# Optimization experiments

Hardware: AMD Instinct MI355X
Metric: run time of the kernel (lower is better)

## Reference

```python
import jax, jax.numpy as jnp
import numpy as np

GROUPS = 4
SF = 2   # scale_factor
K = 3    # filter_k

def conv1x1(x, w, b):
    return jnp.einsum('bchw,oc->bohw', x, w) + b[None, :, None, None]

def grid_sample(img, grid):
    # img: (N,C,H,W); grid: (N,Hg,Wg,2) xy in [-1,1]; bilinear, border padding, align_corners=False
    N, C, H, W = img.shape
    ix = jnp.clip(((grid[..., 0] + 1.0) * W - 1.0) * 0.5, 0.0, W - 1.0)
    iy = jnp.clip(((grid[..., 1] + 1.0) * H - 1.0) * 0.5, 0.0, H - 1.0)
    x0 = jnp.floor(ix); y0 = jnp.floor(iy)
    wx = (ix - x0)[..., None]; wy = (iy - y0)[..., None]
    x0i = x0.astype(jnp.int32); y0i = y0.astype(jnp.int32)
    x1i = jnp.minimum(x0i + 1, W - 1); y1i = jnp.minimum(y0i + 1, H - 1)
    bidx = jnp.arange(N)[:, None, None]
    v00 = img[bidx, :, y0i, x0i]; v01 = img[bidx, :, y0i, x1i]
    v10 = img[bidx, :, y1i, x0i]; v11 = img[bidx, :, y1i, x1i]   # (N,Hg,Wg,C)
    out = (v00 * (1 - wx) * (1 - wy) + v01 * wx * (1 - wy)
           + v10 * (1 - wx) * wy + v11 * wx * wy)
    return jnp.transpose(out, (0, 3, 1, 2))

def def_sample(x, off):
    b, c, h, w = x.shape
    g = GROUPS
    off = off.reshape(b * g, SF, SF, 2, h, w).transpose(0, 4, 1, 5, 2, 3)
    hd, wd = SF * h, SF * w
    off = off.reshape(b * g, hd, wd, 2)
    gy, gx = jnp.meshgrid(jnp.arange(hd, dtype=x.dtype) + 0.5,
                          jnp.arange(wd, dtype=x.dtype) + 0.5, indexing='ij')
    base = jnp.stack([gx, gy], axis=-1)[None]
    grid = 2.0 * (base + off) / jnp.array([wd, hd], dtype=x.dtype) - 1.0
    return grid_sample(x.reshape(b * g, c // g, h, w), grid).reshape(b, c, hd, wd)

def dyn_filter(x, compress, kw, kb):
    b, c, h, w = x.shape
    kern = jax.nn.softmax(conv1x1(compress, kw, kb), axis=1)  # (b,K*K,h,w)
    p = K // 2
    xp = jnp.pad(x, ((0, 0), (0, 0), (p, p), (p, p)))
    patches = jnp.stack([xp[:, :, dy:dy + h, dx:dx + w]
                         for dy in range(K) for dx in range(K)], axis=2)  # (b,c,K*K,h,w)
    return jnp.einsum('bkhw,bckhw->bchw', kern, patches)

def trim_op(x, toff):
    b, c, h, w = x.shape
    g = GROUPS
    off = toff.reshape(b, g, 2, h, w).transpose(0, 1, 3, 4, 2)  # (b,g,h,w,2) xy
    gy, gx = jnp.meshgrid(jnp.arange(h, dtype=x.dtype) + 0.5,
                          jnp.arange(w, dtype=x.dtype) + 0.5, indexing='ij')
    base = jnp.stack([gx, gy], axis=-1)[None, None]
    grid = (2.0 * (base + off) / jnp.array([w, h], dtype=x.dtype) - 1.0).reshape(b * g, h, w, 2)
    return grid_sample(x.reshape(b * g, c // g, h, w), grid).reshape(b, c, h, w)

def setup_inputs():
    key = jax.random.key(0)
    ks = jax.random.split(key, 13)
    C = 256
    oc = GROUPS * SF * SF * 2  # 32
    f = jnp.float32
    return {
        "x": jax.random.normal(ks[0], (4, C, 64, 64), f),
        "def_off_w": jax.random.normal(ks[1], (oc, C), f) * 0.001,
        "def_off_b": jnp.zeros((oc,), f),
        "def_ast_w": jax.random.normal(ks[2], (oc, C), f) * 0.01,
        "def_ast_b": jnp.zeros((oc,), f),
        "comp_w": jax.random.normal(ks[3], (64, C), f) * (1.0 / np.sqrt(C).astype(np.float32)),
        "comp_b": jnp.zeros((64,), f),
        "filt_w": jax.random.normal(ks[4], (K * K, 64), f) * 0.001,
        "filt_b": jnp.zeros((K * K,), f),
        "trim_w": jax.random.normal(ks[5], (GROUPS * 2, 64), f) * 0.001,
        "trim_b": jnp.zeros((GROUPS * 2,), f),
        "trim_ast_w": jax.random.normal(ks[6], (GROUPS * 2, 64), f) * 0.01,
        "trim_ast_b": jnp.zeros((GROUPS * 2,), f),
    }

def reference(x, def_off_w, def_off_b, def_ast_w, def_ast_b, comp_w, comp_b,
              filt_w, filt_b, trim_w, trim_b, trim_ast_w, trim_ast_b):
    off = conv1x1(x, def_off_w, def_off_b) * jax.nn.sigmoid(conv1x1(x, def_ast_w, def_ast_b))
    x_up = def_sample(x, off)                              # (b,c,2h,2w)
    comp = conv1x1(x_up, comp_w, comp_b)                   # (b,64,2h,2w)
    x_filt = dyn_filter(x_up, comp, filt_w, filt_b)
    toff = conv1x1(comp, trim_w, trim_b) * jax.nn.sigmoid(conv1x1(comp, trim_ast_w, trim_ast_b))
    return trim_op(x_filt, toff)
```

## Files before the change

### kernel.cpp

```cpp
#include <hip/hip_runtime.h>
#include <hip/hip_bf16.h>
#include <string.h>

typedef __hip_bfloat16 bf16;
typedef __attribute__((ext_vector_type(8))) short short8;
typedef __attribute__((ext_vector_type(4))) short short4v;
typedef __attribute__((ext_vector_type(4))) float f32x4;

__device__ __forceinline__ float b2f(bf16 v) { return __bfloat162float(v); }
__device__ __forceinline__ bf16  f2b(float v) { return __float2bfloat16(v); }
__device__ __forceinline__ float s2f(short s) {
    return __uint_as_float(((unsigned)(unsigned short)s) << 16);
}
__device__ __forceinline__ short f2s(float v) {
    bf16 t = f2b(v); short s; __builtin_memcpy(&s, &t, 2); return s;
}

#define HWD 16384

__global__ __launch_bounds__(512) void k01_xpose_off(const float* __restrict__ x,
        const float* __restrict__ w_off, const float* __restrict__ b_off,
        const float* __restrict__ w_ast, const float* __restrict__ b_ast,
        bf16* __restrict__ xpm, float* __restrict__ offpm)
{
    __shared__ __align__(16) short tileS[64 * 256];
    const int b = blockIdx.x >> 6;
    const int p0 = (blockIdx.x & 63) << 6;
    const int lane = threadIdx.x & 63;
    const int wave = threadIdx.x >> 6;
    const int n = lane & 15, quad = lane >> 4;
    const int wq = wave & 3;
    const int mh = wave >> 2;

    const int j = (wq << 4) + n, oc = j >> 1, kind = j & 1;
    short8 bfrag[8];
    const float* wrow = (kind ? w_ast : w_off) + oc * 256 + quad * 8;
#pragma unroll
    for (int kc = 0; kc < 8; ++kc) {
        float4 lo = *(const float4*)(wrow + kc * 32);
        float4 hi = *(const float4*)(wrow + kc * 32 + 4);
        short8 f;
        f[0] = f2s(lo.x); f[1] = f2s(lo.y); f[2] = f2s(lo.z); f[3] = f2s(lo.w);
        f[4] = f2s(hi.x); f[5] = f2s(hi.y); f[6] = f2s(hi.z); f[7] = f2s(hi.w);
        bfrag[kc] = f;
    }
    float bias = kind ? b_ast[oc] : b_off[oc];

    {
        const float* xb = x + ((size_t)b << 20);
        const int lp = lane;
#pragma unroll
        for (int gg = 0; gg < 4; ++gg) {
            int cbase = (wave << 5) + (gg << 3);
            short8 pk;
#pragma unroll
            for (int jj = 0; jj < 8; ++jj)
                pk[jj] = f2s(xb[((size_t)(cbase + jj) << 12) + p0 + lp]);
            int slot = (cbase >> 3) ^ (lp & 7);
            *(short8*)&tileS[(lp << 8) + (slot << 3)] = pk;
        }
    }
    __syncthreads();

    {
        short* ob = (short*)xpm + ((size_t)((b << 12) + p0) << 8);
#pragma unroll
        for (int rr = 0; rr < 8; ++rr) {
            int r = (wave << 3) + rr;
            short4v v = *(const short4v*)&tileS[(r << 8)
                        + ((((lane >> 1) ^ (r & 7)) << 3) | ((lane & 1) << 2))];
            *(short4v*)(ob + ((size_t)r << 8) + (lane << 2)) = v;
        }
    }

    float* obase = offpm + ((size_t)(b << 12) << 5);
    f32x4 acc0 = {0.f, 0.f, 0.f, 0.f};
    f32x4 acc1 = {0.f, 0.f, 0.f, 0.f};
#pragma unroll
    for (int kc = 0; kc < 8; ++kc) {
        int slot = (((kc << 2) + quad) ^ (n & 7)) << 3;
        short8 a0 = *(const short8*)&tileS[((mh * 32 + n) << 8) + slot];
        short8 a1 = *(const short8*)&tileS[((mh * 32 + 16 + n) << 8) + slot];
        acc0 = __builtin_amdgcn_mfma_f32_16x16x32_bf16(a0, bfrag[kc], acc0, 0, 0, 0);
        acc1 = __builtin_amdgcn_mfma_f32_16x16x32_bf16(a1, bfrag[kc], acc1, 0, 0, 0);
    }
#pragma unroll
    for (int r = 0; r < 4; ++r) {
        float v0 = acc0[r] + bias;
        float v1 = acc1[r] + bias;
        float p0v = __shfl_xor(v0, 1, 64);
        float p1v = __shfl_xor(v1, 1, 64);
        if (!(n & 1)) {
            int px = p0 + mh * 32 + quad * 4 + r;
            obase[((size_t)px << 5) + oc] = v0 * (1.f / (1.f + expf(-p0v)));
            obase[((size_t)(px + 16) << 5) + oc] = v1 * (1.f / (1.f + expf(-p1v)));
        }
    }
}

__global__ __launch_bounds__(256, 2) void k234_defsample_comp_filter(
        const bf16* __restrict__ xpm, const float* __restrict__ offpm,
        const float* __restrict__ cw, const float* __restrict__ cb,
        const float* __restrict__ fw_g, const float* __restrict__ fb,
        const float* __restrict__ tw, const float* __restrict__ tb,
        const float* __restrict__ taw, const float* __restrict__ tab,
        bf16* __restrict__ xfilt, float* __restrict__ toff)
{
    __shared__ __align__(16) short xupS[100 * 256];
    __shared__ __align__(16) float smc[64][65];
    __shared__ __align__(16) float fwS[64 * 12];
    __shared__ __align__(16) float swS[64 * 16];
    __shared__ __align__(16) short kernS[64][18];

    for (int i = threadIdx.x; i < 64 * 12; i += 256) {
        int c = i / 12, k = i % 12;
        fwS[i] = (k < 9) ? fw_g[k * 64 + c] : 0.f;
    }
    for (int i = threadIdx.x; i < 64 * 16; i += 256) {
        int c = i >> 4, jj = i & 15;
        int oc = jj >> 1, kind = jj & 1;
        swS[i] = kind ? taw[oc * 64 + c] : tw[oc * 64 + c];
    }

    const int b = blockIdx.x >> 8;
    const int tile = blockIdx.x & 255;
    const int ty = tile >> 4, tx = tile & 15;
    const int lane = threadIdx.x & 63;
    const int wave = threadIdx.x >> 6;
    const int n = lane & 15, quad = lane >> 4;
    const int ocb = wave << 4;

    short8 bfrag[8];
    const float* wrow = cw + (ocb + n) * 256 + quad * 8;
#pragma unroll
    for (int kc = 0; kc < 8; ++kc) {
        float4 lo = *(const float4*)(wrow + kc * 32);
        float4 hi = *(const float4*)(wrow + kc * 32 + 4);
        short8 f;
        f[0] = f2s(lo.x); f[1] = f2s(lo.y); f[2] = f2s(lo.z); f[3] = f2s(lo.w);
        f[4] = f2s(hi.x); f[5] = f2s(hi.y); f[6] = f2s(hi.z); f[7] = f2s(hi.w);
        bfrag[kc] = f;
    }
    float bias = cb[ocb + n];

    {
        const short* xsrc = (const short*)xpm + ((size_t)b << 20);
        const int e = lane << 2;
        const int g = lane >> 4;
#pragma unroll 5
        for (int i = 0; i < 25; ++i) {
            int l = wave * 25 + i;
            int lhy = (l * 205) >> 11;
            int lwx = l - lhy * 10;
            int hy = ty * 8 - 1 + lhy;  hy = min(max(hy, 0), 127);
            int wx = tx * 8 - 1 + lwx;  wx = min(max(wx, 0), 127);
            int h = hy >> 1, w = wx >> 1;
            int och = (g << 3) + ((hy & 1) << 2) + ((wx & 1) << 1);
            const float* orow = offpm + ((size_t)((b << 12) + (h << 6) + w) << 5);
            float ox = orow[och], oy = orow[och + 1];
            float ix = (wx + 0.5f + ox) * 0.5f - 0.5f;
            float iy = (hy + 0.5f + oy) * 0.5f - 0.5f;
            ix = fminf(fmaxf(ix, 0.f), 63.f);
            iy = fminf(fmaxf(iy, 0.f), 63.f);
            float x0f = floorf(ix), y0f = floorf(iy);
            float fx = ix - x0f, fy = iy - y0f;
            int x0 = (int)x0f, y0 = (int)y0f;
            int x1 = min(x0 + 1, 63), y1 = min(y0 + 1, 63);
            float w00 = (1.f - fx) * (1.f - fy), w01 = fx * (1.f - fy);
            float w10 = (1.f - fx) * fy,        w11 = fx * fy;
            short4v v00 = *(const short4v*)(xsrc + (((size_t)(y0 << 6) + x0) << 8) + e);
            short4v v01 = *(const short4v*)(xsrc + (((size_t)(y0 << 6) + x1) << 8) + e);
            short4v v10 = *(const short4v*)(xsrc + (((size_t)(y1 << 6) + x0) << 8) + e);
            short4v v11 = *(const short4v*)(xsrc + (((size_t)(y1 << 6) + x1) << 8) + e);
            short4v pk;
#pragma unroll
            for (int jj = 0; jj < 4; ++jj) {
                float v = w00 * s2f(v00[jj]) + w01 * s2f(v01[jj])
                        + w10 * s2f(v10[jj]) + w11 * s2f(v11[jj]);
                pk[jj] = f2s(v);
            }
            *(short4v*)&xupS[(l << 8)
                    + ((((e >> 3) ^ (l & 7)) << 3) | (e & 4))] = pk;
        }
    }
    __syncthreads();

    const int r0 = (((     n) >> 3) + 1) * 10 + (n & 7) + 1;
    const int r1 = (((16 + n) >> 3) + 1) * 10 + (n & 7) + 1;
    const int r2 = (((32 + n) >> 3) + 1) * 10 + (n & 7) + 1;
    const int r3 = (((48 + n) >> 3) + 1) * 10 + (n & 7) + 1;
    f32x4 accA0 = {0.f,0.f,0.f,0.f}, accA1 = {0.f,0.f,0.f,0.f};
    f32x4 accB0 = {0.f,0.f,0.f,0.f}, accB1 = {0.f,0.f,0.f,0.f};
#pragma unroll
    for (int kc = 0; kc < 8; ++kc) {
        int sp = (kc << 2) + quad;
        short8 a0 = *(const short8*)&xupS[(r0 << 8) + ((sp ^ (r0 & 7)) << 3)];
        short8 a1 = *(const short8*)&xupS[(r1 << 8) + ((sp ^ (r1 & 7)) << 3)];
        short8 a2 = *(const short8*)&xupS[(r2 << 8) + ((sp ^ (r2 & 7)) << 3)];
        short8 a3 = *(const short8*)&xupS[(r3 << 8) + ((sp ^ (r3 & 7)) << 3)];
        accA0 = __builtin_amdgcn_mfma_f32_16x16x32_bf16(a0, bfrag[kc], accA0, 0, 0, 0);
        accA1 = __builtin_amdgcn_mfma_f32_16x16x32_bf16(a1, bfrag[kc], accA1, 0, 0, 0);
        accB0 = __builtin_amdgcn_mfma_f32_16x16x32_bf16(a2, bfrag[kc], accB0, 0, 0, 0);
        accB1 = __builtin_amdgcn_mfma_f32_16x16x32_bf16(a3, bfrag[kc], accB1, 0, 0, 0);
    }
#pragma unroll
    for (int r = 0; r < 4; ++r) {
        smc[     quad * 4 + r][ocb + n] = accA0[r] + bias;
        smc[16 + quad * 4 + r][ocb + n] = accA1[r] + bias;
        smc[32 + quad * 4 + r][ocb + n] = accB0[r] + bias;
        smc[48 + quad * 4 + r][ocb + n] = accB1[r] + bias;
    }
    __syncthreads();

    const int px = threadIdx.x & 63;
    const int q = threadIdx.x >> 6;
    if (q == 0) {
        float a[9];
#pragma unroll
        for (int k = 0; k < 9; ++k) a[k] = fb[k];
        for (int c = 0; c < 64; ++c) {
            float v = smc[px][c];
            const float4* wr = reinterpret_cast<const float4*>(&fwS[c * 12]);
            float4 w0 = wr[0], w1 = wr[1];
            float w8 = fwS[c * 12 + 8];
            a[0] += v * w0.x; a[1] += v * w0.y; a[2] += v * w0.z; a[3] += v * w0.w;
            a[4] += v * w1.x; a[5] += v * w1.y; a[6] += v * w1.z; a[7] += v * w1.w;
            a[8] += v * w8;
        }
        float mx = a[0];
#pragma unroll
        for (int k = 1; k < 9; ++k) mx = fmaxf(mx, a[k]);
        float s = 0.f;
#pragma unroll
        for (int k = 0; k < 9; ++k) { a[k] = expf(a[k] - mx); s += a[k]; }
        float inv = 1.f / s;
#pragma unroll
        for (int k = 0; k < 9; ++k) kernS[px][k] = f2s(a[k] * inv);
    } else {
        const int oc0 = (q == 3) ? 6 : (q - 1) * 3;
        const int noc = (q == 3) ? 2 : 3;
        float o[3], aa[3];
        for (int i = 0; i < noc; ++i) { o[i] = tb[oc0 + i]; aa[i] = tab[oc0 + i]; }
        for (int c = 0; c < 64; ++c) {
            float v = smc[px][c];
            const float* wr = &swS[c << 4];
#pragma unroll 3
            for (int i = 0; i < noc; ++i) {
                o[i]  += v * wr[2 * (oc0 + i)];
                aa[i] += v * wr[2 * (oc0 + i) + 1];
            }
        }
        int hw = ((ty * 8 + (px >> 3)) << 7) + tx * 8 + (px & 7);
        for (int i = 0; i < noc; ++i)
            toff[((size_t)((b << 3) + oc0 + i) << 14) + hw] =
                o[i] * (1.f / (1.f + expf(-aa[i])));
    }
    __syncthreads();

    {
        const int chunk = threadIdx.x & 31;
        const int pxg = threadIdx.x >> 5;
#pragma unroll
        for (int it = 0; it < 8; ++it) {
            int p = (pxg << 3) + it;
            int ly = p >> 3, lx = p & 7;
            int gh = ty * 8 + ly, gw = tx * 8 + lx;
            float wk[9];
            short8 k8 = *(const short8*)&kernS[p][0];
#pragma unroll
            for (int k = 0; k < 8; ++k) wk[k] = s2f(k8[k]);
            wk[8] = s2f(kernS[p][8]);
            float ymask[3] = { gh > 0 ? 1.f : 0.f, 1.f, gh < 127 ? 1.f : 0.f };
            float xmask[3] = { gw > 0 ? 1.f : 0.f, 1.f, gw < 127 ? 1.f : 0.f };
            float sum[8];
#pragma unroll
            for (int jj = 0; jj < 8; ++jj) sum[jj] = 0.f;
#pragma unroll
            for (int dy = 0; dy < 3; ++dy) {
#pragma unroll
                for (int dx = 0; dx < 3; ++dx) {
                    float wgt = wk[dy * 3 + dx] * ymask[dy] * xmask[dx];
                    int r = (ly + dy) * 10 + lx + dx;
                    short8 v = *(const short8*)&xupS[(r << 8)
                                + (((chunk ^ (r & 7))) << 3)];
#pragma unroll
                    for (int jj = 0; jj < 8; ++jj) sum[jj] += wgt * s2f(v[jj]);
                }
            }
            short8 pk;
#pragma unroll
            for (int jj = 0; jj < 8; ++jj) pk[jj] = f2s(sum[jj]);
            int hw = (gh << 7) + gw;
            *(short8*)((short*)xfilt + ((size_t)((b << 14) + hw) << 8)
                       + chunk * 8) = pk;
        }
    }
}

__global__ __launch_bounds__(256) void k6_trim(const bf16* __restrict__ xfilt,
        const float* __restrict__ toff, float* __restrict__ out)
{
    __shared__ float sm[32][260];
    int b = blockIdx.x >> 9;
    int hw0 = (blockIdx.x & 511) << 5;
    int wave = threadIdx.x >> 6, lane = threadIdx.x & 63;
    int e = lane * 4;
    int g = lane >> 4;
    const short* xb = (const short*)xfilt + ((size_t)(b * HWD) << 8);
    const float* tfx = toff + ((size_t)(b * 8 + 2 * g)     << 14);
    const float* tfy = toff + ((size_t)(b * 8 + 2 * g + 1) << 14);

    for (int i = 0; i < 8; ++i) {
        int pp = wave * 8 + i;
        int hw = hw0 + pp;
        int h = hw >> 7, w = hw & 127;
        float ox = tfx[hw], oy = tfy[hw];
        float ix = fminf(fmaxf(w + ox, 0.f), 127.f);
        float iy = fminf(fmaxf(h + oy, 0.f), 127.f);
        float x0f = floorf(ix), y0f = floorf(iy);
        float fx = ix - x0f, fy = iy - y0f;
        int x0 = (int)x0f, y0 = (int)y0f;
        int x1 = min(x0 + 1, 127), y1 = min(y0 + 1, 127);
        float w00 = (1.f - fx) * (1.f - fy), w01 = fx * (1.f - fy);
        float w10 = (1.f - fx) * fy,        w11 = fx * fy;
        short4v v00 = *(const short4v*)(xb + (((size_t)(y0 << 7) + x0) << 8) + e);
        short4v v01 = *(const short4v*)(xb + (((size_t)(y0 << 7) + x1) << 8) + e);
        short4v v10 = *(const short4v*)(xb + (((size_t)(y1 << 7) + x0) << 8) + e);
        short4v v11 = *(const short4v*)(xb + (((size_t)(y1 << 7) + x1) << 8) + e);
#pragma unroll
        for (int j = 0; j < 4; ++j) {
            sm[pp][e + j] = w00 * s2f(v00[j]) + w01 * s2f(v01[j])
                          + w10 * s2f(v10[j]) + w11 * s2f(v11[j]);
        }
    }
    __syncthreads();
    int lp = threadIdx.x & 31;
    int c0 = (threadIdx.x >> 5) << 5;
    float* ob = out + (((size_t)b << 8) << 14) + hw0 + lp;
#pragma unroll 8
    for (int k = 0; k < 32; ++k) {
        int c = c0 + k;
        ob[(size_t)c << 14] = sm[lp][c];
    }
}

extern "C" void kernel_launch(void* const* d_in, const int* in_sizes, int n_in,
                              void* d_out, int out_size, void* d_ws, size_t ws_size,
                              hipStream_t stream)
{
    const float* x       = (const float*)d_in[0];
    const float* w_off   = (const float*)d_in[1];
    const float* b_off   = (const float*)d_in[2];
    const float* w_ast   = (const float*)d_in[3];
    const float* b_ast   = (const float*)d_in[4];
    const float* comp_w  = (const float*)d_in[5];
    const float* comp_b  = (const float*)d_in[6];
    const float* filt_w  = (const float*)d_in[7];
    const float* filt_b  = (const float*)d_in[8];
    const float* trim_w  = (const float*)d_in[9];
    const float* trim_b  = (const float*)d_in[10];
    const float* trim_aw = (const float*)d_in[11];
    const float* trim_ab = (const float*)d_in[12];
    float* out = (float*)d_out;

    char* ws = (char*)d_ws;
    float* offpm = (float*)(ws);
    bf16*  xpm   = (bf16*) (ws + (2ull << 20));
    bf16*  xfilt = (bf16*) (ws + (16ull << 20));
    float* toff  = (float*)(ws + (48ull << 20));

    hipLaunchKernelGGL(k01_xpose_off, dim3(256),  dim3(512), 0, stream,
                       x, w_off, b_off, w_ast, b_ast, xpm, offpm);
    hipLaunchKernelGGL(k234_defsample_comp_filter, dim3(1024), dim3(256), 0, stream,
                       xpm, offpm, comp_w, comp_b, filt_w, filt_b,
                       trim_w, trim_b, trim_aw, trim_ab, xfilt, toff);
    hipLaunchKernelGGL(k6_trim,     dim3(2048),  dim3(256), 0, stream,
                       xfilt, toff, out);
}
```

Before: 177.1 us.

## Double block size to 512 threads and widen bilinear gathers to 16 bytes

The fused sample/comp/filter kernel and the trim kernel now launch 512 threads per block instead of 256. Work is split so each wave covers half the MFMA pixel rows, toff is computed by four waves with two channels each, and the filter loop does half as many pixels per thread. The bilinear gathers in both kernels load 8 bf16 channels per lane with 16-byte vector loads, and results go to LDS with wider stores. The goal is more latency hiding and fewer memory instructions, at the cost of higher register pressure per block under the new launch bounds.

```diff
diff --git a/kernel.cpp b/kernel.cpp
--- a/kernel.cpp
+++ b/kernel.cpp
@@ -7,13 +7,11 @@
 typedef __attribute__((ext_vector_type(4))) short short4v;
 typedef __attribute__((ext_vector_type(4))) float f32x4;
 
-__device__ __forceinline__ float b2f(bf16 v) { return __bfloat162float(v); }
-__device__ __forceinline__ bf16  f2b(float v) { return __float2bfloat16(v); }
 __device__ __forceinline__ float s2f(short s) {
     return __uint_as_float(((unsigned)(unsigned short)s) << 16);
 }
 __device__ __forceinline__ short f2s(float v) {
-    bf16 t = f2b(v); short s; __builtin_memcpy(&s, &t, 2); return s;
+    bf16 t = __float2bfloat16(v); short s; __builtin_memcpy(&s, &t, 2); return s;
 }
 
 #define HWD 16384
@@ -98,7 +96,7 @@
     }
 }
 
-__global__ __launch_bounds__(256, 2) void k234_defsample_comp_filter(
+__global__ __launch_bounds__(512, 4) void k234_defsample_comp_filter(
         const bf16* __restrict__ xpm, const float* __restrict__ offpm,
         const float* __restrict__ cw, const float* __restrict__ cb,
         const float* __restrict__ fw_g, const float* __restrict__ fb,
@@ -110,13 +108,13 @@
     __shared__ __align__(16) float smc[64][65];
     __shared__ __align__(16) float fwS[64 * 12];
     __shared__ __align__(16) float swS[64 * 16];
-    __shared__ __align__(16) short kernS[64][18];
-
-    for (int i = threadIdx.x; i < 64 * 12; i += 256) {
+    __shared__ __align__(16) short kernS[64][24];
+
+    for (int i = threadIdx.x; i < 64 * 12; i += 512) {
         int c = i / 12, k = i % 12;
         fwS[i] = (k < 9) ? fw_g[k * 64 + c] : 0.f;
     }
-    for (int i = threadIdx.x; i < 64 * 16; i += 256) {
+    for (int i = threadIdx.x; i < 64 * 16; i += 512) {
         int c = i >> 4, jj = i & 15;
         int oc = jj >> 1, kind = jj & 1;
         swS[i] = kind ? taw[oc * 64 + c] : tw[oc * 64 + c];
@@ -128,7 +126,8 @@
     const int lane = threadIdx.x & 63;
     const int wave = threadIdx.x >> 6;
     const int n = lane & 15, quad = lane >> 4;
-    const int ocb = wave << 4;
+    const int wq = wave & 3, mh = wave >> 2;
+    const int ocb = wq << 4;
 
     short8 bfrag[8];
     const float* wrow = cw + (ocb + n) * 256 + quad * 8;
@@ -145,11 +144,11 @@
 
     {
         const short* xsrc = (const short*)xpm + ((size_t)b << 20);
-        const int e = lane << 2;
-        const int g = lane >> 4;
-#pragma unroll 5
-        for (int i = 0; i < 25; ++i) {
-            int l = wave * 25 + i;
+        const int ph = lane >> 5;
+        const int cl = lane & 31;
+        const int e = cl << 3;
+        const int g = cl >> 3;
+        for (int l = (wave << 1) + ph; l < 100; l += 16) {
             int lhy = (l * 205) >> 11;
             int lwx = l - lhy * 10;
             int hy = ty * 8 - 1 + lhy;  hy = min(max(hy, 0), 127);
@@ -168,52 +167,45 @@
             int x1 = min(x0 + 1, 63), y1 = min(y0 + 1, 63);
             float w00 = (1.f - fx) * (1.f - fy), w01 = fx * (1.f - fy);
             float w10 = (1.f - fx) * fy,        w11 = fx * fy;
-            short4v v00 = *(const short4v*)(xsrc + (((size_t)(y0 << 6) + x0) << 8) + e);
-            short4v v01 = *(const short4v*)(xsrc + (((size_t)(y0 << 6) + x1) << 8) + e);
-            short4v v10 = *(const short4v*)(xsrc + (((size_t)(y1 << 6) + x0) << 8) + e);
-            short4v v11 = *(const short4v*)(xsrc + (((size_t)(y1 << 6) + x1) << 8) + e);
-            short4v pk;
-#pragma unroll
-            for (int jj = 0; jj < 4; ++jj) {
+            short8 v00 = *(const short8*)(xsrc + (((size_t)(y0 << 6) + x0) << 8) + e);
+            short8 v01 = *(const short8*)(xsrc + (((size_t)(y0 << 6) + x1) << 8) + e);
+            short8 v10 = *(const short8*)(xsrc + (((size_t)(y1 << 6) + x0) << 8) + e);
+            short8 v11 = *(const short8*)(xsrc + (((size_t)(y1 << 6) + x1) << 8) + e);
+            short8 pk;
+#pragma unroll
+            for (int jj = 0; jj < 8; ++jj) {
                 float v = w00 * s2f(v00[jj]) + w01 * s2f(v01[jj])
                         + w10 * s2f(v10[jj]) + w11 * s2f(v11[jj]);
                 pk[jj] = f2s(v);
             }
-            *(short4v*)&xupS[(l << 8)
-                    + ((((e >> 3) ^ (l & 7)) << 3) | (e & 4))] = pk;
-        }
-    }
-    __syncthreads();
-
-    const int r0 = (((     n) >> 3) + 1) * 10 + (n & 7) + 1;
-    const int r1 = (((16 + n) >> 3) + 1) * 10 + (n & 7) + 1;
-    const int r2 = (((32 + n) >> 3) + 1) * 10 + (n & 7) + 1;
-    const int r3 = (((48 + n) >> 3) + 1) * 10 + (n & 7) + 1;
-    f32x4 accA0 = {0.f,0.f,0.f,0.f}, accA1 = {0.f,0.f,0.f,0.f};
-    f32x4 accB0 = {0.f,0.f,0.f,0.f}, accB1 = {0.f,0.f,0.f,0.f};
+            int slot = cl ^ (l & 7);
+            *(short8*)&xupS[(l << 8) + (slot << 3)] = pk;
+        }
+    }
+    __syncthreads();
+
+    const int m0 = mh << 5;
+    const int pA = m0 + n, pB = m0 + 16 + n;
+    const int rA = ((pA >> 3) + 1) * 10 + (pA & 7) + 1;
+    const int rB = ((pB >> 3) + 1) * 10 + (pB & 7) + 1;
+    f32x4 acc0 = {0.f,0.f,0.f,0.f}, acc1 = {0.f,0.f,0.f,0.f};
 #pragma unroll
     for (int kc = 0; kc < 8; ++kc) {
         int sp = (kc << 2) + quad;
-        short8 a0 = *(const short8*)&xupS[(r0 << 8) + ((sp ^ (r0 & 7)) << 3)];
-        short8 a1 = *(const short8*)&xupS[(r1 << 8) + ((sp ^ (r1 & 7)) << 3)];
-        short8 a2 = *(const short8*)&xupS[(r2 << 8) + ((sp ^ (r2 & 7)) << 3)];
-        short8 a3 = *(const short8*)&xupS[(r3 << 8) + ((sp ^ (r3 & 7)) << 3)];
-        accA0 = __builtin_amdgcn_mfma_f32_16x16x32_bf16(a0, bfrag[kc], accA0, 0, 0, 0);
-        accA1 = __builtin_amdgcn_mfma_f32_16x16x32_bf16(a1, bfrag[kc], accA1, 0, 0, 0);
-        accB0 = __builtin_amdgcn_mfma_f32_16x16x32_bf16(a2, bfrag[kc], accB0, 0, 0, 0);
-        accB1 = __builtin_amdgcn_mfma_f32_16x16x32_bf16(a3, bfrag[kc], accB1, 0, 0, 0);
+        short8 a0 = *(const short8*)&xupS[(rA << 8) + ((sp ^ (rA & 7)) << 3)];
+        short8 a1 = *(const short8*)&xupS[(rB << 8) + ((sp ^ (rB & 7)) << 3)];
+        acc0 = __builtin_amdgcn_mfma_f32_16x16x32_bf16(a0, bfrag[kc], acc0, 0, 0, 0);
+        acc1 = __builtin_amdgcn_mfma_f32_16x16x32_bf16(a1, bfrag[kc], acc1, 0, 0, 0);
     }
 #pragma unroll
     for (int r = 0; r < 4; ++r) {
-        smc[     quad * 4 + r][ocb + n] = accA0[r] + bias;
-        smc[16 + quad * 4 + r][ocb + n] = accA1[r] + bias;
-        smc[32 + quad * 4 + r][ocb + n] = accB0[r] + bias;
-        smc[48 + quad * 4 + r][ocb + n] = accB1[r] + bias;
-    }
-    __syncthreads();
-
-    const int px = threadIdx.x & 63;
-    const int q = threadIdx.x >> 6;
+        smc[m0 +      quad * 4 + r][ocb + n] = acc0[r] + bias;
+        smc[m0 + 16 + quad * 4 + r][ocb + n] = acc1[r] + bias;
+    }
+    __syncthreads();
+
+    const int px = lane;
+    const int q = wave;
     if (q == 0) {
         float a[9];
 #pragma unroll
@@ -236,22 +228,23 @@
         float inv = 1.f / s;
 #pragma unroll
         for (int k = 0; k < 9; ++k) kernS[px][k] = f2s(a[k] * inv);
-    } else {
-        const int oc0 = (q == 3) ? 6 : (q - 1) * 3;
-        const int noc = (q == 3) ? 2 : 3;
-        float o[3], aa[3];
-        for (int i = 0; i < noc; ++i) { o[i] = tb[oc0 + i]; aa[i] = tab[oc0 + i]; }
+    } else if (q <= 4) {
+        const int oc0 = (q - 1) << 1;
+        float o[2], aa[2];
+#pragma unroll
+        for (int i = 0; i < 2; ++i) { o[i] = tb[oc0 + i]; aa[i] = tab[oc0 + i]; }
         for (int c = 0; c < 64; ++c) {
             float v = smc[px][c];
             const float* wr = &swS[c << 4];
-#pragma unroll 3
-            for (int i = 0; i < noc; ++i) {
+#pragma unroll
+            for (int i = 0; i < 2; ++i) {
                 o[i]  += v * wr[2 * (oc0 + i)];
                 aa[i] += v * wr[2 * (oc0 + i) + 1];
             }
         }
         int hw = ((ty * 8 + (px >> 3)) << 7) + tx * 8 + (px & 7);
-        for (int i = 0; i < noc; ++i)
+#pragma unroll
+        for (int i = 0; i < 2; ++i)
             toff[((size_t)((b << 3) + oc0 + i) << 14) + hw] =
                 o[i] * (1.f / (1.f + expf(-aa[i])));
     }
@@ -261,8 +254,8 @@
         const int chunk = threadIdx.x & 31;
         const int pxg = threadIdx.x >> 5;
 #pragma unroll
-        for (int it = 0; it < 8; ++it) {
-            int p = (pxg << 3) + it;
+        for (int it = 0; it < 4; ++it) {
+            int p = (pxg << 2) + it;
             int ly = p >> 3, lx = p & 7;
             int gh = ty * 8 + ly, gw = tx * 8 + lx;
             float wk[9];
@@ -297,21 +290,24 @@
     }
 }
 
-__global__ __launch_bounds__(256) void k6_trim(const bf16* __restrict__ xfilt,
+__global__ __launch_bounds__(512, 4) void k6_trim(const bf16* __restrict__ xfilt,
         const float* __restrict__ toff, float* __restrict__ out)
 {
-    __shared__ float sm[32][260];
+    __shared__ __align__(16) float sm[32][260];
     int b = blockIdx.x >> 9;
     int hw0 = (blockIdx.x & 511) << 5;
     int wave = threadIdx.x >> 6, lane = threadIdx.x & 63;
-    int e = lane * 4;
-    int g = lane >> 4;
+    int ph = lane >> 5;
+    int cl = lane & 31;
+    int e = cl << 3;
+    int g = cl >> 3;
     const short* xb = (const short*)xfilt + ((size_t)(b * HWD) << 8);
     const float* tfx = toff + ((size_t)(b * 8 + 2 * g)     << 14);
     const float* tfy = toff + ((size_t)(b * 8 + 2 * g + 1) << 14);
 
-    for (int i = 0; i < 8; ++i) {
-        int pp = wave * 8 + i;
+#pragma unroll
+    for (int i = 0; i < 2; ++i) {
+        int pp = (wave << 2) + (i << 1) + ph;
         int hw = hw0 + pp;
         int h = hw >> 7, w = hw & 127;
         float ox = tfx[hw], oy = tfy[hw];
@@ -323,23 +319,29 @@
         int x1 = min(x0 + 1, 127), y1 = min(y0 + 1, 127);
         float w00 = (1.f - fx) * (1.f - fy), w01 = fx * (1.f - fy);
         float w10 = (1.f - fx) * fy,        w11 = fx * fy;
-        short4v v00 = *(const short4v*)(xb + (((size_t)(y0 << 7) + x0) << 8) + e);
-        short4v v01 = *(const short4v*)(xb + (((size_t)(y0 << 7) + x1) << 8) + e);
-        short4v v10 = *(const short4v*)(xb + (((size_t)(y1 << 7) + x0) << 8) + e);
-        short4v v11 = *(const short4v*)(xb + (((size_t)(y1 << 7) + x1) << 8) + e);
-#pragma unroll
-        for (int j = 0; j < 4; ++j) {
-            sm[pp][e + j] = w00 * s2f(v00[j]) + w01 * s2f(v01[j])
-                          + w10 * s2f(v10[j]) + w11 * s2f(v11[j]);
-        }
+        short8 v00 = *(const short8*)(xb + (((size_t)(y0 << 7) + x0) << 8) + e);
+        short8 v01 = *(const short8*)(xb + (((size_t)(y0 << 7) + x1) << 8) + e);
+        short8 v10 = *(const short8*)(xb + (((size_t)(y1 << 7) + x0) << 8) + e);
+        short8 v11 = *(const short8*)(xb + (((size_t)(y1 << 7) + x1) << 8) + e);
+        float4 lo, hi;
+        lo.x = w00 * s2f(v00[0]) + w01 * s2f(v01[0]) + w10 * s2f(v10[0]) + w11 * s2f(v11[0]);
+        lo.y = w00 * s2f(v00[1]) + w01 * s2f(v01[1]) + w10 * s2f(v10[1]) + w11 * s2f(v11[1]);
+        lo.z = w00 * s2f(v00[2]) + w01 * s2f(v01[2]) + w10 * s2f(v10[2]) + w11 * s2f(v11[2]);
+        lo.w = w00 * s2f(v00[3]) + w01 * s2f(v01[3]) + w10 * s2f(v10[3]) + w11 * s2f(v11[3]);
+        hi.x = w00 * s2f(v00[4]) + w01 * s2f(v01[4]) + w10 * s2f(v10[4]) + w11 * s2f(v11[4]);
+        hi.y = w00 * s2f(v00[5]) + w01 * s2f(v01[5]) + w10 * s2f(v10[5]) + w11 * s2f(v11[5]);
+        hi.z = w00 * s2f(v00[6]) + w01 * s2f(v01[6]) + w10 * s2f(v10[6]) + w11 * s2f(v11[6]);
+        hi.w = w00 * s2f(v00[7]) + w01 * s2f(v01[7]) + w10 * s2f(v10[7]) + w11 * s2f(v11[7]);
+        *(float4*)&sm[pp][e]     = lo;
+        *(float4*)&sm[pp][e + 4] = hi;
     }
     __syncthreads();
     int lp = threadIdx.x & 31;
-    int c0 = (threadIdx.x >> 5) << 5;
-    float* ob = out + (((size_t)b << 8) << 14) + hw0 + lp;
+    int cg = threadIdx.x >> 5;
+    float* ob = out + ((size_t)b << 22) + hw0 + lp;
 #pragma unroll 8
-    for (int k = 0; k < 32; ++k) {
-        int c = c0 + k;
+    for (int k = 0; k < 16; ++k) {
+        int c = (cg << 4) + k;
         ob[(size_t)c << 14] = sm[lp][c];
     }
 }
@@ -371,9 +373,9 @@
 
     hipLaunchKernelGGL(k01_xpose_off, dim3(256),  dim3(512), 0, stream,
                        x, w_off, b_off, w_ast, b_ast, xpm, offpm);
-    hipLaunchKernelGGL(k234_defsample_comp_filter, dim3(1024), dim3(256), 0, stream,
+    hipLaunchKernelGGL(k234_defsample_comp_filter, dim3(1024), dim3(512), 0, stream,
                        xpm, offpm, comp_w, comp_b, filt_w, filt_b,
                        trim_w, trim_b, trim_aw, trim_ab, xfilt, toff);
-    hipLaunchKernelGGL(k6_trim,     dim3(2048),  dim3(256), 0, stream,
+    hipLaunchKernelGGL(k6_trim,     dim3(2048),  dim3(512), 0, stream,
                        xfilt, toff, out);
 }
```

After: 170.4 us. 3.8% less time.
